# Kernel tuning notes

Measured on AMD Instinct MI355X. Metric: run time of the kernel, lower is better.

Reference implementation:

```python
import jax, jax.numpy as jnp
import numpy as np

N_NODES = 50000
N_EDGES = 800000
IN_F = 128
OUT_F = 128
HEADS = 8
HEAD_DIM = OUT_F // HEADS
EDGE_F = 64


def setup_inputs() -> dict:
    key = jax.random.key(0)
    ks = jax.random.split(key, 12)
    s = 0.05
    return {
        "node_features": jax.random.normal(ks[0], (N_NODES, IN_F), jnp.float32),
        "edge_index": jax.random.randint(ks[1], (2, N_EDGES), 0, N_NODES, jnp.int32),
        "edge_features": jax.random.normal(ks[2], (N_EDGES, EDGE_F), jnp.float32),
        "Wq": jax.random.normal(ks[3], (IN_F, OUT_F), jnp.float32) * s,
        "bq": jnp.zeros((OUT_F,), jnp.float32),
        "Wk": jax.random.normal(ks[4], (IN_F, OUT_F), jnp.float32) * s,
        "bk": jnp.zeros((OUT_F,), jnp.float32),
        "Wv": jax.random.normal(ks[5], (IN_F, OUT_F), jnp.float32) * s,
        "bv": jnp.zeros((OUT_F,), jnp.float32),
        "We": jax.random.normal(ks[6], (EDGE_F, HEADS), jnp.float32) * s,
        "be": jnp.zeros((HEADS,), jnp.float32),
        "Wo": jax.random.normal(ks[7], (OUT_F, OUT_F), jnp.float32) * s,
        "bo": jnp.zeros((OUT_F,), jnp.float32),
    }


def reference(node_features, edge_index, edge_features,
              Wq, bq, Wk, bk, Wv, bv, We, be, Wo, bo):
    n_nodes = node_features.shape[0]
    scale = HEAD_DIM ** (-0.5)
    sources = edge_index[0]
    targets = edge_index[1]

    q = (node_features @ Wq + bq).reshape(n_nodes, HEADS, HEAD_DIM)
    k = (node_features @ Wk + bk).reshape(n_nodes, HEADS, HEAD_DIM)
    v = (node_features @ Wv + bv).reshape(n_nodes, HEADS, HEAD_DIM)

    # edge-wise gathers: [E, H, D]
    q_t = q[targets]
    k_s = k[sources]
    v_s = v[sources]

    # scores [E, H] with edge bias
    scores = jnp.sum(q_t * k_s, axis=-1) * scale + (edge_features @ We + be)

    # segment softmax over edges sharing a target node
    max_s = jax.ops.segment_max(scores, targets, num_segments=n_nodes)
    e = jnp.exp(scores - max_s[targets])
    denom = jax.ops.segment_sum(e, targets, num_segments=n_nodes) + 1e-10
    probs = e / denom[targets]

    weighted = (probs[:, :, None] * v_s).reshape(scores.shape[0], -1)  # [E, H*D]
    agg = jax.ops.segment_sum(weighted, targets, num_segments=n_nodes)  # [N, H*D]
    return agg @ Wo + bo
```

## Files before the change

kernel.cpp:

```cpp
#include <hip/hip_runtime.h>
#include <hip/hip_bf16.h>
#include <math.h>

#define IN_F   128
#define OUT_F  128
#define HEADS  8
#define HEAD_D 16
#define EDGE_F 64
#define BUCKET 64

typedef __attribute__((ext_vector_type(8))) short bf16x8;
typedef __attribute__((ext_vector_type(4))) float f32x4;

__device__ inline unsigned int f2bf(float f) {
    union { float f; unsigned int u; } c; c.f = f;
    unsigned int r = c.u + 0x7FFFu + ((c.u >> 16) & 1u);
    return r >> 16;
}

__device__ inline int wperm(int col) {
    return (col & 0x70) | ((col & 7) << 1) | ((col >> 3) & 1);
}

__global__ __launch_bounds__(256)
void prep_kernel(const float* __restrict__ Wq, const float* __restrict__ Wk,
                 const float* __restrict__ Wv, const float* __restrict__ Wo,
                 uint4* __restrict__ Wb, int* __restrict__ deg, int n_nodes) {
    int id = blockIdx.x * 256 + threadIdx.x;
    if (id < n_nodes) deg[id] = 0;
    if (id >= 8192) return;
    int lane = id & 63;
    int kb   = (id >> 6) & 3;
    int ct   = (id >> 8) & 7;
    int mat  = id >> 11;
    const float* W = (mat == 0) ? Wq : (mat == 1) ? Wk : (mat == 2) ? Wv : Wo;
    int n  = ct * 16 + (lane & 15);
    int k0 = kb * 32 + (lane >> 4) * 8;
    unsigned int t[8];
    #pragma unroll
    for (int j = 0; j < 8; ++j) t[j] = f2bf(W[(size_t)(k0 + j) * 128 + n]);
    uint4 val;
    val.x = t[0] | (t[1] << 16);
    val.y = t[2] | (t[3] << 16);
    val.z = t[4] | (t[5] << 16);
    val.w = t[6] | (t[7] << 16);
    Wb[id] = val;
}

__global__ __launch_bounds__(256)
void qkv_edges(const float* __restrict__ x, const bf16x8* __restrict__ WbV,
               const float* __restrict__ bq, const float* __restrict__ bk,
               const float* __restrict__ bv,
               float* __restrict__ q, unsigned int* __restrict__ kvp, int n_nodes,
               const float* __restrict__ ef, const float* __restrict__ We,
               const float* __restrict__ be, float* __restrict__ ebias_csr,
               const int* __restrict__ ei, int* __restrict__ deg,
               int* __restrict__ csr_src, int n_edges, int node_blocks) {
    __shared__ float sWe[EDGE_F * 9];
    __shared__ float sbe[HEADS];
    const int tid = threadIdx.x;

    if ((int)blockIdx.x < node_blocks) {
        const int wave = tid >> 6;
        const int lane = tid & 63;
        const int quad = lane >> 4;
        const int lcol = lane & 15;
        const int row0 = blockIdx.x * 64 + wave * 16;
        const int m    = row0 + lcol;

        bf16x8 afrag[4];
        const bool mv = (m < n_nodes);
        const float* xr = x + (size_t)m * IN_F;
        #pragma unroll
        for (int kb = 0; kb < 4; ++kb) {
            float buf[8];
            if (mv) {
                float4 a = ((const float4*)(xr + kb * 32 + quad * 8))[0];
                float4 b = ((const float4*)(xr + kb * 32 + quad * 8 + 4))[0];
                buf[0]=a.x; buf[1]=a.y; buf[2]=a.z; buf[3]=a.w;
                buf[4]=b.x; buf[5]=b.y; buf[6]=b.z; buf[7]=b.w;
            } else {
                #pragma unroll
                for (int j = 0; j < 8; ++j) buf[j] = 0.f;
            }
            bf16x8 f;
            #pragma unroll
            for (int j = 0; j < 8; ++j) f[j] = (short)f2bf(buf[j]);
            afrag[kb] = f;
        }

        #pragma unroll
        for (int ct = 0; ct < 8; ++ct) {
            f32x4 aq = {0.f,0.f,0.f,0.f}, ak = {0.f,0.f,0.f,0.f}, av = {0.f,0.f,0.f,0.f};
            #pragma unroll
            for (int kb = 0; kb < 4; ++kb) {
                bf16x8 bq_ = WbV[((0 * 8 + ct) * 4 + kb) * 64 + lane];
                bf16x8 bk_ = WbV[((1 * 8 + ct) * 4 + kb) * 64 + lane];
                bf16x8 bv_ = WbV[((2 * 8 + ct) * 4 + kb) * 64 + lane];
                aq = __builtin_amdgcn_mfma_f32_16x16x32_bf16(afrag[kb], bq_, aq, 0, 0, 0);
                ak = __builtin_amdgcn_mfma_f32_16x16x32_bf16(afrag[kb], bk_, ak, 0, 0, 0);
                av = __builtin_amdgcn_mfma_f32_16x16x32_bf16(afrag[kb], bv_, av, 0, 0, 0);
            }
            const int col = ct * 16 + lcol;
            const int wcol = wperm(col);
            float bqc = bq[col], bkc = bk[col], bvc = bv[col];
            #pragma unroll
            for (int r = 0; r < 4; ++r) {
                int node = row0 + quad * 4 + r;
                if (node < n_nodes) {
                    q[(size_t)node * OUT_F + col]    = aq[r] + bqc;
                    kvp[(size_t)node * OUT_F + wcol] = f2bf(ak[r] + bkc) | (f2bf(av[r] + bvc) << 16);
                }
            }
        }
    } else {
        #pragma unroll
        for (int i = tid; i < EDGE_F * HEADS; i += 256)
            sWe[(i >> 3) * 9 + (i & 7)] = We[i];
        if (tid < HEADS) sbe[tid] = be[tid];
        __syncthreads();

        const int wave = tid >> 6;
        const int lane = tid & 63;
        const int g    = lane >> 3;
        const int c    = lane & 7;
        const int e    = (blockIdx.x - node_blocks) * 32 + wave * 8 + g;
        const bool ok  = (e < n_edges);

        float4 a = make_float4(0.f,0.f,0.f,0.f), b = a;
        if (ok) {
            const float4* er = (const float4*)(ef + (size_t)e * EDGE_F + c * 8);
            a = er[0]; b = er[1];
        }

        int t_ = 0, pos = BUCKET;
        if (ok && c == 0) {
            int s_ = ei[e];
            t_ = ei[n_edges + e];
            pos = atomicAdd(&deg[t_], 1);
            if (pos < BUCKET) csr_src[((size_t)t_ << 6) + pos] = s_;
        }

        float acc[HEADS];
        #pragma unroll
        for (int h = 0; h < HEADS; ++h) acc[h] = 0.f;
        float evv[8] = {a.x, a.y, a.z, a.w, b.x, b.y, b.z, b.w};
        #pragma unroll
        for (int jj = 0; jj < 8; ++jj) {
            #pragma unroll
            for (int h = 0; h < HEADS; ++h)
                acc[h] = fmaf(evv[jj], sWe[(c * 8 + jj) * 9 + h], acc[h]);
        }
        #pragma unroll
        for (int m = 1; m < 8; m <<= 1) {
            #pragma unroll
            for (int h = 0; h < HEADS; ++h)
                acc[h] += __shfl_xor(acc[h], m, 8);
        }
        int slot = __shfl(pos, lane & 56);
        int tb   = __shfl(t_,  lane & 56);
        if (ok && slot < BUCKET)
            ebias_csr[(((size_t)tb << 6) + slot) * HEADS + c] = acc[c] + sbe[c];
    }
}

__global__ __launch_bounds__(256)
void agg_kernel(const int* __restrict__ csr_src, const int* __restrict__ deg,
                const float* __restrict__ q, const unsigned long long* __restrict__ kvpu,
                const float* __restrict__ ebias_csr, unsigned short* __restrict__ aggn,
                int n_nodes) {
    const int tid  = threadIdx.x;
    const int wave = tid >> 6;
    const int lane = tid & 63;
    const int t    = blockIdx.x * 4 + wave;
    if (t >= n_nodes) return;

    const int h  = lane >> 3;
    const int r  = lane & 7;
    const int fa = h * 16 + r;

    const float qa = q[(size_t)t * OUT_F + fa];
    const float qb = q[(size_t)t * OUT_F + fa + 8];

    const int beg = t << 6;
    int cnt = deg[t]; if (cnt > BUCKET) cnt = BUCKET;

    const int csrv = csr_src[beg + lane];

    float acc_a = 0.f, acc_b = 0.f, den = 0.f;

    auto process = [&](unsigned long long kv, float eb) {
        unsigned int w0 = (unsigned int)kv;
        unsigned int w1 = (unsigned int)(kv >> 32);
        float ka = __uint_as_float(w0 << 16);
        float va = __uint_as_float(w0 & 0xFFFF0000u);
        float kb = __uint_as_float(w1 << 16);
        float vb = __uint_as_float(w1 & 0xFFFF0000u);
        float pa = __fmul_rn(qa, ka);
        float pb = __fmul_rn(qb, kb);
        float p  = __fadd_rn(pa, pb);
        p = __fadd_rn(p, __shfl_xor(p, 4, 8));
        p = __fadd_rn(p, __shfl_xor(p, 2, 8));
        p = __fadd_rn(p, __shfl_xor(p, 1, 8));
        float w = __expf(fmaf(p, 0.25f, eb));
        den += w;
        acc_a = fmaf(w, va, acc_a);
        acc_b = fmaf(w, vb, acc_b);
    };

    unsigned long long kv[8]; float eb[8];
    #pragma unroll
    for (int j = 0; j < 8; ++j) {
        kv[j] = 0; eb[j] = 0.f;
        if (j < cnt) {
            int src = __shfl(csrv, j);
            kv[j] = kvpu[(size_t)src * 64 + lane];
            eb[j] = ebias_csr[(size_t)(beg + j) * HEADS + h];
        }
    }

    int i = 0;
    while (i + 8 <= cnt) {
        unsigned long long nkv[8]; float neb[8];
        #pragma unroll
        for (int j = 0; j < 8; ++j) {
            nkv[j] = 0; neb[j] = 0.f;
            if (i + 8 + j < cnt) {
                int src = __shfl(csrv, i + 8 + j);
                nkv[j] = kvpu[(size_t)src * 64 + lane];
                neb[j] = ebias_csr[(size_t)(beg + i + 8 + j) * HEADS + h];
            }
        }
        #pragma unroll
        for (int j = 0; j < 8; ++j) process(kv[j], eb[j]);
        #pragma unroll
        for (int j = 0; j < 8; ++j) { kv[j] = nkv[j]; eb[j] = neb[j]; }
        i += 8;
    }
    #pragma unroll
    for (int j = 0; j < 8; ++j)
        if (i + j < cnt) process(kv[j], eb[j]);

    float d = den + 1e-10f;
    aggn[(size_t)t * OUT_F + fa]     = (unsigned short)f2bf(acc_a / d);
    aggn[(size_t)t * OUT_F + fa + 8] = (unsigned short)f2bf(acc_b / d);
}

__global__ __launch_bounds__(256)
void out_mfma(const unsigned short* __restrict__ aggn, const bf16x8* __restrict__ WbV,
              const float* __restrict__ bo, float* __restrict__ out, int n_nodes) {
    const int tid  = threadIdx.x;
    const int wave = tid >> 6;
    const int lane = tid & 63;
    const int quad = lane >> 4;
    const int lcol = lane & 15;
    const int row0 = blockIdx.x * 64 + wave * 16;
    const int m    = row0 + lcol;

    bf16x8 afrag[4];
    const bool mv = (m < n_nodes);
    const bf16x8* ar = (const bf16x8*)(aggn + (size_t)m * OUT_F);
    #pragma unroll
    for (int kb = 0; kb < 4; ++kb) {
        if (mv) afrag[kb] = ar[kb * 4 + quad];
        else {
            bf16x8 z;
            #pragma unroll
            for (int j = 0; j < 8; ++j) z[j] = 0;
            afrag[kb] = z;
        }
    }

    #pragma unroll
    for (int ct = 0; ct < 8; ++ct) {
        f32x4 acc = {0.f, 0.f, 0.f, 0.f};
        #pragma unroll
        for (int kb = 0; kb < 4; ++kb) {
            bf16x8 b = WbV[((3 * 8 + ct) * 4 + kb) * 64 + lane];
            acc = __builtin_amdgcn_mfma_f32_16x16x32_bf16(afrag[kb], b, acc, 0, 0, 0);
        }
        const int col = ct * 16 + lcol;
        float boc = bo[col];
        #pragma unroll
        for (int r = 0; r < 4; ++r) {
            int node = row0 + quad * 4 + r;
            if (node < n_nodes) out[(size_t)node * OUT_F + col] = acc[r] + boc;
        }
    }
}

extern "C" void kernel_launch(void* const* d_in, const int* in_sizes, int n_in,
                              void* d_out, int out_size, void* d_ws, size_t ws_size,
                              hipStream_t stream) {
    const float* x  = (const float*)d_in[0];
    const int*   ei = (const int*)  d_in[1];
    const float* ef = (const float*)d_in[2];
    const float* Wq = (const float*)d_in[3];
    const float* bq = (const float*)d_in[4];
    const float* Wk = (const float*)d_in[5];
    const float* bk = (const float*)d_in[6];
    const float* Wv = (const float*)d_in[7];
    const float* bv = (const float*)d_in[8];
    const float* We = (const float*)d_in[9];
    const float* be = (const float*)d_in[10];
    const float* Wo = (const float*)d_in[11];
    const float* bo = (const float*)d_in[12];
    float* out = (float*)d_out;

    const int n_nodes = in_sizes[0] / IN_F;
    const int n_edges = in_sizes[1] / 2;

    char* w = (char*)d_ws;
    float*          q       = (float*)w;          w += (size_t)n_nodes * OUT_F * 4;
    unsigned int*   kvp     = (unsigned int*)w;   w += (size_t)n_nodes * OUT_F * 4;
    unsigned short* aggn    = (unsigned short*)w; w += (size_t)n_nodes * OUT_F * 2;
    uint4*          Wb      = (uint4*)w;          w += (size_t)8192 * 16;
    int*            deg     = (int*)w;            w += (size_t)n_nodes * 4;
    int*            csr_src = (int*)w;            w += (size_t)n_nodes * BUCKET * 4;
    float*          ebias_csr = (float*)w;

    {
        int threads_needed = (n_nodes > 8192) ? n_nodes : 8192;
        prep_kernel<<<(threads_needed + 255) / 256, 256, 0, stream>>>(
            Wq, Wk, Wv, Wo, Wb, deg, n_nodes);
    }

    {
        int node_blocks = (n_nodes + 63) / 64;
        int edge_blocks = (n_edges + 31) / 32;
        qkv_edges<<<node_blocks + edge_blocks, 256, 0, stream>>>(
            x, (const bf16x8*)Wb, bq, bk, bv, q, kvp, n_nodes,
            ef, We, be, ebias_csr, ei, deg, csr_src, n_edges, node_blocks);
    }

    agg_kernel<<<(n_nodes + 3) / 4, 256, 0, stream>>>(
        csr_src, deg, q, (const unsigned long long*)kvp, ebias_csr, aggn, n_nodes);

    out_mfma<<<(n_nodes + 63) / 64, 256, 0, stream>>>(
        aggn, (const bf16x8*)Wb, bo, out, n_nodes);
}
```

Before: 563.5 us.

## Store edge bias per edge and record edge id in CSR buckets

The edge-bias kernel now writes the bias in original edge order as contiguous float2 stores. It no longer scatters it into the CSR bucket slot, which needed shuffles to broadcast slot and target. The CSR entry becomes an int2 holding the source and the edge id, and the aggregation kernel gathers the bias through the edge id. Each lane now handles 16 edge features instead of 8, so a block covers 64 edges. The cost is more CSR traffic and a random gather of edge bias in the aggregation step.

```diff
diff --git a/kernel.cpp b/kernel.cpp
--- a/kernel.cpp
+++ b/kernel.cpp
@@ -53,9 +53,9 @@
                const float* __restrict__ bv,
                float* __restrict__ q, unsigned int* __restrict__ kvp, int n_nodes,
                const float* __restrict__ ef, const float* __restrict__ We,
-               const float* __restrict__ be, float* __restrict__ ebias_csr,
+               const float* __restrict__ be, float* __restrict__ ebias,
                const int* __restrict__ ei, int* __restrict__ deg,
-               int* __restrict__ csr_src, int n_edges, int node_blocks) {
+               int2* __restrict__ csr2, int n_edges, int node_blocks) {
     __shared__ float sWe[EDGE_F * 9];
     __shared__ float sbe[HEADS];
     const int tid = threadIdx.x;
@@ -122,52 +122,54 @@
 
         const int wave = tid >> 6;
         const int lane = tid & 63;
-        const int g    = lane >> 3;
-        const int c    = lane & 7;
-        const int e    = (blockIdx.x - node_blocks) * 32 + wave * 8 + g;
+        const int g    = lane >> 2;
+        const int c    = lane & 3;
+        const int e    = (blockIdx.x - node_blocks) * 64 + wave * 16 + g;
         const bool ok  = (e < n_edges);
 
-        float4 a = make_float4(0.f,0.f,0.f,0.f), b = a;
+        float4 a0, a1, a2, a3;
+        a0 = a1 = a2 = a3 = make_float4(0.f, 0.f, 0.f, 0.f);
         if (ok) {
-            const float4* er = (const float4*)(ef + (size_t)e * EDGE_F + c * 8);
-            a = er[0]; b = er[1];
-        }
-
-        int t_ = 0, pos = BUCKET;
+            const float4* er = (const float4*)(ef + (size_t)e * EDGE_F + c * 16);
+            a0 = er[0]; a1 = er[1]; a2 = er[2]; a3 = er[3];
+        }
+
         if (ok && c == 0) {
             int s_ = ei[e];
-            t_ = ei[n_edges + e];
-            pos = atomicAdd(&deg[t_], 1);
-            if (pos < BUCKET) csr_src[((size_t)t_ << 6) + pos] = s_;
+            int t_ = ei[n_edges + e];
+            int pos = atomicAdd(&deg[t_], 1);
+            if (pos < BUCKET) csr2[((size_t)t_ << 6) + pos] = make_int2(s_, e);
         }
 
         float acc[HEADS];
         #pragma unroll
         for (int h = 0; h < HEADS; ++h) acc[h] = 0.f;
-        float evv[8] = {a.x, a.y, a.z, a.w, b.x, b.y, b.z, b.w};
-        #pragma unroll
-        for (int jj = 0; jj < 8; ++jj) {
+        float evv[16] = {a0.x, a0.y, a0.z, a0.w, a1.x, a1.y, a1.z, a1.w,
+                         a2.x, a2.y, a2.z, a2.w, a3.x, a3.y, a3.z, a3.w};
+        #pragma unroll
+        for (int jj = 0; jj < 16; ++jj) {
             #pragma unroll
             for (int h = 0; h < HEADS; ++h)
-                acc[h] = fmaf(evv[jj], sWe[(c * 8 + jj) * 9 + h], acc[h]);
-        }
-        #pragma unroll
-        for (int m = 1; m < 8; m <<= 1) {
+                acc[h] = fmaf(evv[jj], sWe[(c * 16 + jj) * 9 + h], acc[h]);
+        }
+        #pragma unroll
+        for (int m = 1; m < 4; m <<= 1) {
             #pragma unroll
             for (int h = 0; h < HEADS; ++h)
-                acc[h] += __shfl_xor(acc[h], m, 8);
-        }
-        int slot = __shfl(pos, lane & 56);
-        int tb   = __shfl(t_,  lane & 56);
-        if (ok && slot < BUCKET)
-            ebias_csr[(((size_t)tb << 6) + slot) * HEADS + c] = acc[c] + sbe[c];
+                acc[h] += __shfl_xor(acc[h], m, 4);
+        }
+        if (ok) {
+            float2 st = make_float2(acc[2 * c]     + sbe[2 * c],
+                                    acc[2 * c + 1] + sbe[2 * c + 1]);
+            ((float2*)(ebias + (size_t)e * HEADS))[c] = st;
+        }
     }
 }
 
 __global__ __launch_bounds__(256)
-void agg_kernel(const int* __restrict__ csr_src, const int* __restrict__ deg,
+void agg_kernel(const int2* __restrict__ csr2, const int* __restrict__ deg,
                 const float* __restrict__ q, const unsigned long long* __restrict__ kvpu,
-                const float* __restrict__ ebias_csr, unsigned short* __restrict__ aggn,
+                const float* __restrict__ ebias, unsigned short* __restrict__ aggn,
                 int n_nodes) {
     const int tid  = threadIdx.x;
     const int wave = tid >> 6;
@@ -185,7 +187,7 @@
     const int beg = t << 6;
     int cnt = deg[t]; if (cnt > BUCKET) cnt = BUCKET;
 
-    const int csrv = csr_src[beg + lane];
+    const int2 csrv = csr2[beg + lane];
 
     float acc_a = 0.f, acc_b = 0.f, den = 0.f;
 
@@ -213,9 +215,10 @@
     for (int j = 0; j < 8; ++j) {
         kv[j] = 0; eb[j] = 0.f;
         if (j < cnt) {
-            int src = __shfl(csrv, j);
+            int src = __shfl(csrv.x, j);
+            int eid = __shfl(csrv.y, j);
             kv[j] = kvpu[(size_t)src * 64 + lane];
-            eb[j] = ebias_csr[(size_t)(beg + j) * HEADS + h];
+            eb[j] = ebias[(size_t)eid * HEADS + h];
         }
     }
 
@@ -226,9 +229,10 @@
         for (int j = 0; j < 8; ++j) {
             nkv[j] = 0; neb[j] = 0.f;
             if (i + 8 + j < cnt) {
-                int src = __shfl(csrv, i + 8 + j);
+                int src = __shfl(csrv.x, i + 8 + j);
+                int eid = __shfl(csrv.y, i + 8 + j);
                 nkv[j] = kvpu[(size_t)src * 64 + lane];
-                neb[j] = ebias_csr[(size_t)(beg + i + 8 + j) * HEADS + h];
+                neb[j] = ebias[(size_t)eid * HEADS + h];
             }
         }
         #pragma unroll
@@ -311,13 +315,13 @@
     const int n_edges = in_sizes[1] / 2;
 
     char* w = (char*)d_ws;
-    float*          q       = (float*)w;          w += (size_t)n_nodes * OUT_F * 4;
-    unsigned int*   kvp     = (unsigned int*)w;   w += (size_t)n_nodes * OUT_F * 4;
-    unsigned short* aggn    = (unsigned short*)w; w += (size_t)n_nodes * OUT_F * 2;
-    uint4*          Wb      = (uint4*)w;          w += (size_t)8192 * 16;
-    int*            deg     = (int*)w;            w += (size_t)n_nodes * 4;
-    int*            csr_src = (int*)w;            w += (size_t)n_nodes * BUCKET * 4;
-    float*          ebias_csr = (float*)w;
+    float*          q     = (float*)w;          w += (size_t)n_nodes * OUT_F * 4;
+    unsigned int*   kvp   = (unsigned int*)w;   w += (size_t)n_nodes * OUT_F * 4;
+    unsigned short* aggn  = (unsigned short*)w; w += (size_t)n_nodes * OUT_F * 2;
+    uint4*          Wb    = (uint4*)w;          w += (size_t)8192 * 16;
+    int*            deg   = (int*)w;            w += (size_t)n_nodes * 4;
+    int2*           csr2  = (int2*)w;           w += (size_t)n_nodes * BUCKET * 8;
+    float*          ebias = (float*)w;
 
     {
         int threads_needed = (n_nodes > 8192) ? n_nodes : 8192;
@@ -327,14 +331,14 @@
 
     {
         int node_blocks = (n_nodes + 63) / 64;
-        int edge_blocks = (n_edges + 31) / 32;
+        int edge_blocks = (n_edges + 63) / 64;
         qkv_edges<<<node_blocks + edge_blocks, 256, 0, stream>>>(
             x, (const bf16x8*)Wb, bq, bk, bv, q, kvp, n_nodes,
-            ef, We, be, ebias_csr, ei, deg, csr_src, n_edges, node_blocks);
+            ef, We, be, ebias, ei, deg, csr2, n_edges, node_blocks);
     }
 
     agg_kernel<<<(n_nodes + 3) / 4, 256, 0, stream>>>(
-        csr_src, deg, q, (const unsigned long long*)kvp, ebias_csr, aggn, n_nodes);
+        csr2, deg, q, (const unsigned long long*)kvp, ebias, aggn, n_nodes);
 
     out_mfma<<<(n_nodes + 63) / 64, 256, 0, stream>>>(
         aggn, (const bf16x8*)Wb, bo, out, n_nodes);
```

After: 519.2 us. -7.9%, faster.
